# Optimization experiments

Measured on AMD Instinct MI355X. Metric: run time of the kernel, lower is better.

The kernel has to match this reference:

```python
import jax, jax.numpy as jnp
import numpy as np

T, B = 1024, 256
N = T * B
D = 128  # d_model
IN = 36  # lstm input size = 16 + 4 + 16


def _w(k, shape, s=0.1):
    return jax.random.normal(k, shape, dtype=jnp.float32) * s


def setup_inputs() -> dict:
    key = jax.random.key(0)
    ks = jax.random.split(key, 32)
    inp = {}
    inp["image"] = jax.random.uniform(ks[0], (N, 1, 3, 3), jnp.float32) * 255.0
    inp["location"] = jax.random.uniform(ks[1], (N, 2), jnp.float32) * 5.0
    inp["message"] = jax.random.randint(ks[2], (N,), 0, 16)
    inp["done"] = (jax.random.uniform(ks[3], (N,)) < 0.05).astype(jnp.float32)
    inp["h0"] = jax.random.normal(ks[4], (1, B, D), jnp.float32)
    inp["c0"] = jax.random.normal(ks[5], (1, B, D), jnp.float32)
    # visual encoder: 9 -> 256 -> 256 -> 128 -> 16 (ReLU each)
    inp["vis_W1"] = _w(ks[6], (256, 9));   inp["vis_b1"] = jnp.zeros((256,), jnp.float32)
    inp["vis_W2"] = _w(ks[7], (256, 256)); inp["vis_b2"] = jnp.zeros((256,), jnp.float32)
    inp["vis_W3"] = _w(ks[8], (128, 256)); inp["vis_b3"] = jnp.zeros((128,), jnp.float32)
    inp["vis_W4"] = _w(ks[9], (16, 128));  inp["vis_b4"] = jnp.zeros((16,), jnp.float32)
    # location encoder: 2 -> 4
    inp["loc_W"] = _w(ks[10], (4, 2)); inp["loc_b"] = jnp.zeros((4,), jnp.float32)
    # message encoder: Embedding(16,16) -> Linear(16,16) -> ReLU
    inp["emb"] = _w(ks[11], (16, 16), 1.0)
    inp["msg_W"] = _w(ks[12], (16, 16)); inp["msg_b"] = jnp.zeros((16,), jnp.float32)
    # LSTM params (torch layout, gate order i,f,g,o)
    inp["W_ih"] = _w(ks[13], (4 * D, IN)); inp["W_hh"] = _w(ks[14], (4 * D, D))
    inp["b_ih"] = jnp.zeros((4 * D,), jnp.float32); inp["b_hh"] = jnp.zeros((4 * D,), jnp.float32)
    # heads
    inp["actor_W"] = _w(ks[15], (5, D), 0.01);   inp["actor_b"] = jnp.zeros((5,), jnp.float32)
    inp["head_W"] = _w(ks[16], (16, D), 0.01);   inp["head_b"] = jnp.zeros((16,), jnp.float32)
    inp["critic_W"] = _w(ks[17], (1, D), 1.0);   inp["critic_b"] = jnp.zeros((1,), jnp.float32)
    return inp


def reference(image, location, message, done, h0, c0,
              vis_W1, vis_b1, vis_W2, vis_b2, vis_W3, vis_b3, vis_W4, vis_b4,
              loc_W, loc_b, emb, msg_W, msg_b,
              W_ih, W_hh, b_ih, b_hh,
              actor_W, actor_b, head_W, head_b, critic_W, critic_b):
    # encoders (all rows at once)
    x = image.reshape(N, -1) / 255.0
    x = jax.nn.relu(x @ vis_W1.T + vis_b1)
    x = jax.nn.relu(x @ vis_W2.T + vis_b2)
    x = jax.nn.relu(x @ vis_W3.T + vis_b3)
    img_feat = jax.nn.relu(x @ vis_W4.T + vis_b4)                 # [N,16]
    loc_feat = (location / 5.0) @ loc_W.T + loc_b                 # [N,4]
    msg_feat = jax.nn.relu(emb[message] @ msg_W.T + msg_b)        # [N,16]
    feat = jnp.concatenate([img_feat, loc_feat, msg_feat], axis=1).reshape(T, B, IN)
    d = done.reshape(T, B)

    def step(carry, inp_t):
        h, c = carry
        x_t, d_t = inp_t
        m = (1.0 - d_t)[:, None]
        h = h * m
        c = c * m
        gates = x_t @ W_ih.T + h @ W_hh.T + (b_ih + b_hh)         # [B,4D]
        i, f, g, o = jnp.split(gates, 4, axis=-1)
        i = jax.nn.sigmoid(i); f = jax.nn.sigmoid(f)
        g = jnp.tanh(g);       o = jax.nn.sigmoid(o)
        c = f * c + i * g
        h = o * jnp.tanh(c)
        return (h, c), h

    (_, _), hs = jax.lax.scan(step, (h0[0], c0[0]), (feat, d))
    hidden = hs.reshape(N, D)
    action_logits = hidden @ actor_W.T + actor_b                  # [N,5]
    message_logits = hidden @ head_W.T + head_b                   # [N,16]
    value = hidden @ critic_W.T + critic_b                        # [N,1]
    return jnp.concatenate([action_logits, message_logits, value], axis=1)  # [N,22]
```

## Files before the change

kernel.cpp:

```cpp
#include <hip/hip_runtime.h>
#include <hip/hip_bf16.h>

#define DEV __device__ __forceinline__

typedef short short8 __attribute__((ext_vector_type(8)));
typedef _Float16 h8 __attribute__((ext_vector_type(8)));
typedef _Float16 h2 __attribute__((ext_vector_type(2)));
typedef float f32x4 __attribute__((ext_vector_type(4)));
typedef unsigned short u16;

constexpr int T_ = 1024, B_ = 256, N_ = T_ * B_, D_ = 128;
constexpr int FS = 48;
constexpr int NSLOT = 16;
constexpr int SEGQC = 64;
constexpr int MAXIT = 392;
constexpr int CH = 48;
constexpr int WARM = 56;
constexpr int MAXPC = 768;
constexpr unsigned DEADT = 0xFFFFu;
constexpr unsigned TRB = 0x10000u;
constexpr unsigned NWB = 0x20000u;

DEV u16 f2b(float f) {
  unsigned u = __float_as_uint(f);
  return (u16)((u + 0x7fffu + ((u >> 16) & 1u)) >> 16);
}

#if __has_builtin(__builtin_amdgcn_exp2f)
#define EXP2F __builtin_amdgcn_exp2f
#else
#define EXP2F __exp2f
#endif
#if __has_builtin(__builtin_amdgcn_rcpf)
#define RCPF __builtin_amdgcn_rcpf
#else
#define RCPF(x) (1.0f / (x))
#endif
DEV float sigf(float x) { return RCPF(1.0f + EXP2F(x * -1.44269504f)); }
DEV float tanhf_(float x) {
  return fmaf(RCPF(1.0f + EXP2F(x * -2.88539008f)), 2.0f, -1.0f);
}

__global__ void prep_kernel(const float* W1, const float* W2, const float* W3,
                            const float* W4, const float* emb, const float* msgW,
                            const float* msgb, const float* Wih, const float* Whh,
                            const float* bih, const float* bhh, const float* aW,
                            const float* ab, const float* hW, const float* hb,
                            const float* cW, const float* cb, u16* w1p, u16* w2b,
                            u16* w3b, u16* w4b, float* msgtab, _Float16* wfull,
                            float* biass, _Float16* w22, float* b22) {
  int i0 = blockIdx.x * blockDim.x + threadIdx.x;
  int st = gridDim.x * blockDim.x;
  for (int i = i0; i < 256 * 32; i += st) {
    int r = i >> 5, k = i & 31;
    w1p[i] = (k < 9) ? f2b(W1[r * 9 + k]) : (u16)0;
  }
  for (int i = i0; i < 256 * 256; i += st) w2b[i] = f2b(W2[i]);
  for (int i = i0; i < 128 * 256; i += st) w3b[i] = f2b(W3[i]);
  for (int i = i0; i < 16 * 128; i += st) w4b[i] = f2b(W4[i]);
  for (int i = i0; i < 256; i += st) {
    int v = i >> 4, j = i & 15;
    float s = msgb[j];
    for (int k = 0; k < 16; ++k) s += emb[v * 16 + k] * msgW[j * 16 + k];
    msgtab[i] = s > 0.f ? s : 0.f;
  }
  for (int i = i0; i < 512 * 192; i += st) {
    int c = i / 192, k = i % 192;
    float v;
    if (k < 128) v = Whh[(size_t)c * 128 + k];
    else {
      int p = k - 128;
      if (p < 18) v = Wih[(size_t)c * 36 + p];
      else if (p >= 24 && p < 42) v = Wih[(size_t)c * 36 + p - 6];
      else v = 0.f;
    }
    wfull[i] = (_Float16)v;
  }
  for (int i = i0; i < 512; i += st) biass[i] = bih[i] + bhh[i];
  for (int i = i0; i < 32 * 128; i += st) {
    int c = i >> 7, k = i & 127;
    float v = 0.f;
    if (c < 5) v = aW[c * 128 + k];
    else if (c < 21) v = hW[(c - 5) * 128 + k];
    else if (c == 21) v = cW[k];
    w22[i] = (_Float16)v;
  }
  for (int i = i0; i < 32; i += st) {
    float v = 0.f;
    if (i < 5) v = ab[i];
    else if (i < 21) v = hb[i - 5];
    else if (i == 21) v = cb[0];
    b22[i] = v;
  }
}

__global__ __launch_bounds__(64) void seg_scan_kernel(const float* done,
                                                      unsigned* segq, int* nq) {
  __shared__ unsigned short brkpos[1024];
  __shared__ int lcnt[64];
  __shared__ int nb_sh;
  __shared__ int pcs[MAXPC];
  __shared__ int np_sh;
  const int b = blockIdx.x;
  const int l = threadIdx.x;

  unsigned mask = 0;
#pragma unroll
  for (int j = 0; j < 16; ++j) {
    const int t = l * 16 + j;
    const float dv = (t == 0) ? 0.0f : done[(size_t)t * B_ + b];
    mask |= (dv != 0.0f) ? (1u << j) : 0u;
  }
  lcnt[l] = __popc(mask);
  __syncthreads();
  if (l == 0) {
    int acc = 0;
    for (int i = 0; i < 64; ++i) { const int c = lcnt[i]; lcnt[i] = acc; acc += c; }
    nb_sh = acc;
  }
  __syncthreads();
  {
    int off = lcnt[l];
    unsigned mm = mask;
    while (mm) {
      const int j = __builtin_ctz(mm);
      mm &= mm - 1;
      brkpos[off++] = (unsigned short)(l * 16 + j);
    }
  }
  __syncthreads();
  if (l == 0) {
    int np = 0;
    const int nb = nb_sh;
    int t0 = 0;
    for (int s = 0; s <= nb; ++s) {
      const int t1 = (s < nb) ? (int)brkpos[s] : T_;
      int k = 0;
      for (int ps = t0; ps < t1 && np < MAXPC; ps += CH, ++k) {
        const int pl = min(CH, t1 - ps);
        const int wl = (k == 0) ? 0 : min(WARM, ps - t0);
        pcs[np++] = ps | (pl << 10) | (wl << 17);
      }
      t0 = t1;
    }
    np_sh = np;
  }
  __syncthreads();
  const int np = np_sh;
  int ssum[16], scnt[16];
#pragma unroll
  for (int j = 0; j < 16; ++j) { ssum[j] = 0; scnt[j] = 0; }
  if (l == 0 && np > 0) {
    const int e = pcs[0];
    segq[((size_t)b * NSLOT + 0) * SEGQC + 0] = (unsigned)e;
    ssum[0] = ((e >> 10) & 127) + ((e >> 17) & 127);
    scnt[0] = 1;
    pcs[0] = -1;
  }
  __syncthreads();
  for (int it = 1; it < np; ++it) {
    int bestw = -1, bestk = 0;
    for (int j = l; j < np; j += 64) {
      const int e = pcs[j];
      if (e >= 0) {
        const int w = ((e >> 10) & 127) + ((e >> 17) & 127);
        if (w > bestw || (w == bestw && j < bestk)) { bestw = w; bestk = j; }
      }
    }
    int pk = (bestw < 0) ? -1 : ((bestw << 10) | (1023 - bestk));
#pragma unroll
    for (int wd = 32; wd >= 1; wd >>= 1) pk = max(pk, __shfl_xor(pk, wd));
    if (l == 0 && pk >= 0) {
      const int k = 1023 - (pk & 1023);
      const int e = pcs[k];
      const int w = pk >> 10;
      int m = 0, best = 0x7fffffff;
#pragma unroll
      for (int j = 0; j < 16; ++j) {
        const int v = (scnt[j] >= SEGQC) ? 0x7fffffff : ssum[j];
        if (v < best) { best = v; m = j; }
      }
      segq[((size_t)b * NSLOT + m) * SEGQC + scnt[m]] = (unsigned)e;
      ssum[m] += w;
      ++scnt[m];
      pcs[k] = -1;
    }
    __syncthreads();
  }
  if (l == 0) {
#pragma unroll
    for (int j = 0; j < 16; ++j) nq[b * NSLOT + j] = scnt[j];
  }
}

__global__ __launch_bounds__(64) void sched_build_kernel(const unsigned* segq,
                                                         const int* nq,
                                                         unsigned* sched,
                                                         int* bsteps) {
  const int b = blockIdx.x;
  const int l = threadIdx.x;
  int it = 0;
  if (l < NSLOT) {
    const int gs = b * NSLOT + l;
    const unsigned* q = segq + (size_t)gs * SEGQC;
    const int cnt = nq[gs];
    unsigned* sc = sched + (size_t)b * MAXIT * 16 + l;
    for (int s = 0; s < cnt; ++s) {
      const unsigned e = q[s];
      const int ps = (int)(e & 1023u);
      const int pl = (int)((e >> 10) & 127u);
      const int wl = (int)((e >> 17) & 127u);
      for (int j = 0; j < wl && it < MAXIT - 8; ++j) {
        sc[(size_t)it * 16] = (unsigned)(ps - wl + j) | NWB;
        ++it;
      }
      for (int j = 0; j < pl && it < MAXIT - 8; ++j) {
        sc[(size_t)it * 16] = (unsigned)(ps + j) | ((j == pl - 1) ? TRB : 0u);
        ++it;
      }
    }
  }
  int mk = (l < NSLOT) ? it : 0;
#pragma unroll
  for (int w = 8; w >= 1; w >>= 1) mk = max(mk, __shfl_xor(mk, w));
  if (l < NSLOT) {
    unsigned* sc = sched + (size_t)b * MAXIT * 16 + l;
    const int pe = min(mk + 8, MAXIT);
    for (int i2 = it; i2 < pe; ++i2) sc[(size_t)i2 * 16] = DEADT | TRB;
    if (l == 0) bsteps[b] = mk;
  }
}

template <int K, int OUTN, bool SWZIN>
DEV void mlp_layer128(const u16* Ain, u16* Aout, const u16* Wb, const float* bias,
                      int mh, int cq, int lane) {
  constexpr int KT = K / 32;
  constexpr int NT = OUTN / 64;
  constexpr int PASSES = NT / 2;
  const int lr = lane & 15, lg = lane >> 4;
  const int colbase = cq * (OUTN / 4);
  const int rowbase = mh * 64;
#pragma unroll
  for (int ps = 0; ps < PASSES; ++ps) {
    short8 bf[2][KT];
    float bcol[2];
#pragma unroll
    for (int n2 = 0; n2 < 2; ++n2) {
      const int col = colbase + (ps * 2 + n2) * 16 + lr;
#pragma unroll
      for (int kt = 0; kt < KT; ++kt)
        bf[n2][kt] = *(const short8*)(Wb + col * K + kt * 32 + lg * 8);
      bcol[n2] = bias[col];
    }
#pragma unroll
    for (int mt = 0; mt < 4; ++mt) {
      const int arow = rowbase + mt * 16 + lr;
      short8 af[KT];
#pragma unroll
      for (int kt = 0; kt < KT; ++kt) {
        int kb = (kt * 32 + lg * 8) * 2;
        if (SWZIN) kb ^= (arow & 7) << 4;
        af[kt] = *(const short8*)(Ain + arow * K + (kb >> 1));
      }
      f32x4 acc[2];
#pragma unroll
      for (int n2 = 0; n2 < 2; ++n2)
        acc[n2] = f32x4{bcol[n2], bcol[n2], bcol[n2], bcol[n2]};
#pragma unroll
      for (int kt = 0; kt < KT; ++kt)
#pragma unroll
        for (int n2 = 0; n2 < 2; ++n2)
          acc[n2] = __builtin_amdgcn_mfma_f32_16x16x32_bf16(af[kt], bf[n2][kt],
                                                            acc[n2], 0, 0, 0);
#pragma unroll
      for (int n2 = 0; n2 < 2; ++n2) {
        const int col = colbase + (ps * 2 + n2) * 16 + lr;
#pragma unroll
        for (int r = 0; r < 4; ++r) {
          const int orow = rowbase + mt * 16 + lg * 4 + r;
          float v = acc[n2][r];
          v = v > 0.f ? v : 0.f;
          const int kb = (col * 2) ^ ((orow & 7) << 4);
          Aout[orow * OUTN + (kb >> 1)] = f2b(v);
        }
      }
    }
  }
}

__global__ __launch_bounds__(512) void enc_kernel(
    const float* image, const float* location, const int* message,
    const float* vb1, const float* vb2, const float* vb3, const float* vb4,
    const float* locW, const float* locb, const u16* w1p, const u16* w2b,
    const u16* w3b, const u16* w4b, const float* msgtab, _Float16* featf) {
  __shared__ __align__(16) u16 bufA[128 * 256];
  __shared__ __align__(16) u16 bufB[128 * 256];
  const int n0 = blockIdx.x * 128;
  const int tid = threadIdx.x;
  const int wave = tid >> 6, lane = tid & 63;
  const int mh = wave >> 2, cq = wave & 3;

  for (int i = tid; i < 128 * 32; i += 512) {
    int r = i >> 5, k = i & 31;
    float v = (k < 9) ? image[(size_t)(n0 + r) * 9 + k] * (1.0f / 255.0f) : 0.0f;
    bufA[i] = f2b(v);
  }
  __syncthreads();
  mlp_layer128<32, 256, false>(bufA, bufB, w1p, vb1, mh, cq, lane);
  __syncthreads();
  mlp_layer128<256, 256, true>(bufB, bufA, w2b, vb2, mh, cq, lane);
  __syncthreads();
  mlp_layer128<256, 128, true>(bufA, bufB, w3b, vb3, mh, cq, lane);
  __syncthreads();
  {
    const int lr = lane & 15, lg = lane >> 4;
    short8 bfr[4];
#pragma unroll
    for (int kt = 0; kt < 4; ++kt)
      bfr[kt] = *(const short8*)(w4b + lr * 128 + kt * 32 + lg * 8);
    const float bcol = vb4[lr];
    f32x4 acc = {bcol, bcol, bcol, bcol};
#pragma unroll
    for (int kt = 0; kt < 4; ++kt) {
      const int arow = wave * 16 + lr;
      const int kb = ((kt * 32 + lg * 8) * 2) ^ ((arow & 7) << 4);
      const short8 af = *(const short8*)(bufB + arow * 128 + (kb >> 1));
      acc = __builtin_amdgcn_mfma_f32_16x16x32_bf16(af, bfr[kt], acc, 0, 0, 0);
    }
#pragma unroll
    for (int r = 0; r < 4; ++r) {
      const int row = wave * 16 + lg * 4 + r;
      float v = acc[r];
      v = v > 0.f ? v : 0.f;
      featf[(size_t)(n0 + row) * FS + lr] = (_Float16)v;
    }
  }
  if (tid < 128) {
    const int n = n0 + tid;
    _Float16* fr = featf + (size_t)n * FS;
#pragma unroll
    for (int j = 0; j < 6; ++j) fr[18 + j] = (_Float16)0.f;
#pragma unroll
    for (int j = 0; j < 6; ++j) fr[42 + j] = (_Float16)0.f;
    const float x0 = location[(size_t)n * 2] * 0.2f;
    const float x1 = location[(size_t)n * 2 + 1] * 0.2f;
#pragma unroll
    for (int j = 0; j < 4; ++j) {
      const int pos = (j < 2) ? 16 + j : 22 + j;
      fr[pos] = (_Float16)fmaf(x0, locW[j * 2], fmaf(x1, locW[j * 2 + 1], locb[j]));
    }
    const float* mrow = msgtab + message[n] * 16;
#pragma unroll
    for (int j = 0; j < 16; ++j) fr[26 + j] = (_Float16)mrow[j];
  }
}

__global__ __launch_bounds__(512, 2) void lstm_seg_kernel(
    const _Float16* featf, const _Float16* wfull, const float* biass,
    const unsigned* sched, const int* bsteps, const float* h0, const float* c0,
    const float* done, _Float16* hidh) {
  __shared__ __align__(16) char abuf[2][16 * 384];
  const int b = blockIdx.x;
  const int tid = threadIdx.x;
  const int wave = tid >> 6, l = tid & 63;
  const int lc = l & 15, lg = l >> 4;
  const int d = wave * 16 + lc;
  const bool fth = (wave < 6) && (lc < 4);
  const int fslot = lg * 4 + lc;
  const int fch = wave;

  h8 bf[4][6];
#pragma unroll
  for (int g = 0; g < 4; ++g) {
    const _Float16* wp = wfull + (size_t)(g * 128 + d) * 192;
#pragma unroll
    for (int kt = 0; kt < 6; ++kt)
      bf[g][kt] = *(const h8*)(wp + kt * 32 + lg * 8);
  }
  float bias4[4];
#pragma unroll
  for (int g = 0; g < 4; ++g) bias4[g] = biass[g * 128 + d];

  for (int i = tid; i < 2 * 16 * 384 / 4; i += 512) ((float*)abuf)[i] = 0.0f;
  __syncthreads();

  const int nsteps = bsteps[b];
  const unsigned* sb = sched + (size_t)b * MAXIT * 16;
  uint4 sr0 = *(const uint4*)(sb + 0 * 16 + lg * 4);
  uint4 sr1 = *(const uint4*)(sb + 1 * 16 + lg * 4);
  unsigned ss1 = DEADT, ss2 = DEADT, t00 = DEADT;
  if (fth) {
    t00 = sb[0 * 16 + fslot] & 0xFFFFu;
    ss1 = sb[1 * 16 + fslot];
    ss2 = sb[2 * 16 + fslot];
  }

  const float m0 = 1.0f - done[b];
  if (tid < 128)
    *(_Float16*)(abuf[0] + 2 * tid) = (_Float16)(h0[(size_t)b * D_ + tid] * m0);
  float creg[4];
#pragma unroll
  for (int r = 0; r < 4; ++r) {
    const int row = lg * 4 + r;
    creg[r] = (row == 0) ? c0[(size_t)b * D_ + d] * m0 : 0.0f;
  }
  if (fth && t00 != DEADT) {
    const unsigned fo = t00 * (unsigned)(B_ * FS) + (unsigned)(b * FS) + fch * 8;
    const uint4 fz = *(const uint4*)(featf + fo);
    const int byte = (fslot * 384 + 256 + fch * 16) ^ ((fslot & 7) << 4);
    *(uint4*)(abuf[0] + byte) = fz;
  }
  uint4 fvW = {0, 0, 0, 0};
  if (fth && (ss1 & 0xFFFFu) != DEADT) {
    const unsigned fo =
        (ss1 & 0xFFFFu) * (unsigned)(B_ * FS) + (unsigned)(b * FS) + fch * 8;
    fvW = *(const uint4*)(featf + fo);
  }
  __syncthreads();

  int p = 0;
  for (int i = 0; i < nsteps; ++i) {
    const uint4 srN = *(const uint4*)(sb + (size_t)(i + 2) * 16 + lg * 4);
    unsigned ssN = DEADT;
    if (fth) ssN = sb[(size_t)(i + 3) * 16 + fslot];
    const char* bp = abuf[p];
    h8 af[6];
#pragma unroll
    for (int kt = 0; kt < 6; ++kt) {
      const int byte = (lc * 384 + ((kt * 32 + lg * 8) << 1)) ^ ((lc & 7) << 4);
      af[kt] = *(const h8*)(bp + byte);
    }
    uint4 fvN = {0, 0, 0, 0};
    const unsigned t2 = ss2 & 0xFFFFu;
    if (fth && t2 != DEADT) {
      const unsigned fo = t2 * (unsigned)(B_ * FS) + (unsigned)(b * FS) + fch * 8;
      fvN = *(const uint4*)(featf + fo);
    }
    f32x4 acc[4];
#pragma unroll
    for (int g = 0; g < 4; ++g)
      acc[g] = f32x4{bias4[g], bias4[g], bias4[g], bias4[g]};
#pragma unroll
    for (int kt = 0; kt < 6; ++kt)
#pragma unroll
      for (int g = 0; g < 4; ++g)
        acc[g] = __builtin_amdgcn_mfma_f32_16x16x32_f16(af[kt], bf[g][kt],
                                                        acc[g], 0, 0, 0);
    char* bn = abuf[p ^ 1];
#pragma unroll
    for (int r = 0; r < 4; ++r) {
      const int row = lg * 4 + r;
      const unsigned e = ((const unsigned*)&sr0)[r];
      const float gi = sigf(acc[0][r]);
      const float gf = sigf(acc[1][r]);
      const float gg = tanhf_(acc[2][r]);
      const float go = sigf(acc[3][r]);
      const float cn = fmaf(gf, creg[r], gi * gg);
      const float hv = go * tanhf_(cn);
      const unsigned tt = e & 0xFFFFu;
      const bool tr = (e & TRB) != 0u;
      creg[r] = tr ? 0.0f : cn;
      *(_Float16*)(bn + ((row * 384 + 2 * d) ^ ((row & 7) << 4))) =
          (_Float16)(tr ? 0.0f : hv);
      if (tt != DEADT && !(e & NWB)) {
        const unsigned ho = (tt << 15) + (unsigned)((b << 7) + d);
        hidh[ho] = (_Float16)hv;
      }
    }
    if (fth && (ss1 & 0xFFFFu) != DEADT) {
      const int byte = (fslot * 384 + 256 + fch * 16) ^ ((fslot & 7) << 4);
      *(uint4*)(bn + byte) = fvW;
    }
    sr0 = sr1; sr1 = srN;
    ss1 = ss2; ss2 = ssN;
    fvW = fvN;
    asm volatile("s_waitcnt lgkmcnt(0)" ::: "memory");
    __builtin_amdgcn_s_barrier();
    p ^= 1;
  }
}

__global__ __launch_bounds__(256) void head_kernel(const _Float16* hidh,
                                                   const _Float16* w22,
                                                   const float* b22, float* out) {
  const int tid = threadIdx.x;
  const int w = tid >> 6, l = tid & 63;
  const int lr = l & 15, lg = l >> 4;
  const int row0 = blockIdx.x * 64 + w * 16;

  h8 bfr[2][4];
#pragma unroll
  for (int ct = 0; ct < 2; ++ct)
#pragma unroll
    for (int kt = 0; kt < 4; ++kt)
      bfr[ct][kt] = *(const h8*)(w22 + (ct * 16 + lr) * 128 + kt * 32 + lg * 8);
  h8 af[4];
#pragma unroll
  for (int kt = 0; kt < 4; ++kt)
    af[kt] = *(const h8*)(hidh + (size_t)(row0 + lr) * D_ + kt * 32 + lg * 8);

  f32x4 acc[2];
#pragma unroll
  for (int ct = 0; ct < 2; ++ct) acc[ct] = f32x4{0.f, 0.f, 0.f, 0.f};
#pragma unroll
  for (int kt = 0; kt < 4; ++kt)
#pragma unroll
    for (int ct = 0; ct < 2; ++ct)
      acc[ct] = __builtin_amdgcn_mfma_f32_16x16x32_f16(af[kt], bfr[ct][kt],
                                                       acc[ct], 0, 0, 0);
#pragma unroll
  for (int ct = 0; ct < 2; ++ct) {
    const int col = ct * 16 + lr;
    if (col < 22) {
      const float bb = b22[col];
#pragma unroll
      for (int r = 0; r < 4; ++r) {
        const int row = row0 + lg * 4 + r;
        out[(size_t)row * 22 + col] = acc[ct][r] + bb;
      }
    }
  }
}

extern "C" void kernel_launch(void* const* d_in, const int* in_sizes, int n_in,
                              void* d_out, int out_size, void* d_ws, size_t ws_size,
                              hipStream_t stream) {
  const float* image = (const float*)d_in[0];
  const float* location = (const float*)d_in[1];
  const int* message = (const int*)d_in[2];
  const float* done = (const float*)d_in[3];
  const float* h0 = (const float*)d_in[4];
  const float* c0 = (const float*)d_in[5];
  const float* vW1 = (const float*)d_in[6];
  const float* vb1 = (const float*)d_in[7];
  const float* vW2 = (const float*)d_in[8];
  const float* vb2 = (const float*)d_in[9];
  const float* vW3 = (const float*)d_in[10];
  const float* vb3 = (const float*)d_in[11];
  const float* vW4 = (const float*)d_in[12];
  const float* vb4 = (const float*)d_in[13];
  const float* locW = (const float*)d_in[14];
  const float* locb = (const float*)d_in[15];
  const float* emb = (const float*)d_in[16];
  const float* msgW = (const float*)d_in[17];
  const float* msgb = (const float*)d_in[18];
  const float* Wih = (const float*)d_in[19];
  const float* Whh = (const float*)d_in[20];
  const float* bih = (const float*)d_in[21];
  const float* bhh = (const float*)d_in[22];
  const float* aW = (const float*)d_in[23];
  const float* ab = (const float*)d_in[24];
  const float* hW = (const float*)d_in[25];
  const float* hb = (const float*)d_in[26];
  const float* cW = (const float*)d_in[27];
  const float* cb = (const float*)d_in[28];

  char* ws = (char*)d_ws;
  size_t off = 0;
  auto alloc = [&](size_t bytes) {
    void* p = ws + off;
    off = (off + bytes + 255) & ~(size_t)255;
    return p;
  };
  _Float16* featf = (_Float16*)alloc((size_t)N_ * FS * 2);
  _Float16* hidh = (_Float16*)alloc((size_t)N_ * D_ * 2);
  u16* w1p = (u16*)alloc(256 * 32 * 2);
  u16* w2b = (u16*)alloc(256 * 256 * 2);
  u16* w3b = (u16*)alloc(128 * 256 * 2);
  u16* w4b = (u16*)alloc(16 * 128 * 2);
  float* msgtab = (float*)alloc(256 * 4);
  _Float16* wfull = (_Float16*)alloc(512 * 192 * 2);
  float* biass = (float*)alloc(512 * 4);
  unsigned* segq = (unsigned*)alloc((size_t)B_ * NSLOT * SEGQC * 4);
  int* nqA = (int*)alloc(B_ * NSLOT * 4);
  unsigned* sched = (unsigned*)alloc((size_t)B_ * MAXIT * 16 * 4);
  int* bsteps = (int*)alloc(B_ * 4);
  _Float16* w22 = (_Float16*)alloc(32 * 128 * 2);
  float* b22 = (float*)alloc(32 * 4);
  (void)in_sizes; (void)n_in; (void)out_size; (void)ws_size;

  prep_kernel<<<128, 256, 0, stream>>>(vW1, vW2, vW3, vW4, emb, msgW, msgb, Wih,
                                       Whh, bih, bhh, aW, ab, hW, hb, cW, cb, w1p,
                                       w2b, w3b, w4b, msgtab, wfull, biass, w22,
                                       b22);
  seg_scan_kernel<<<B_, 64, 0, stream>>>(done, segq, nqA);
  sched_build_kernel<<<B_, 64, 0, stream>>>(segq, nqA, sched, bsteps);
  enc_kernel<<<N_ / 128, 512, 0, stream>>>(image, location, message, vb1, vb2, vb3,
                                           vb4, locW, locb, w1p, w2b, w3b, w4b,
                                           msgtab, featf);
  lstm_seg_kernel<<<B_, 512, 0, stream>>>(featf, wfull, biass, sched, bsteps,
                                          h0, c0, done, hidh);
  head_kernel<<<N_ / 64, 256, 0, stream>>>(hidh, w22, b22, (float*)d_out);
}
```

Baseline: 483.6 us.

## Split visual encoder into two kernels with chunked global intermediate

The single 512-thread encoder kernel, which used 128 KB of LDS per block, is split into two 256-thread kernels over 64-row tiles. Layers 1-2 write a bf16 activation buffer to global memory and layers 3-4 read it back, with the work processed in chunks sized to fit the workspace. The image 1/255 scaling is also folded into the first-layer weights. The aim is to cut LDS per block so more blocks fit per CU, at the cost of an extra global round trip for the 256-wide activations and more kernel launches.

```diff
diff --git a/kernel.cpp b/kernel.cpp
--- a/kernel.cpp
+++ b/kernel.cpp
@@ -53,7 +53,7 @@
   int st = gridDim.x * blockDim.x;
   for (int i = i0; i < 256 * 32; i += st) {
     int r = i >> 5, k = i & 31;
-    w1p[i] = (k < 9) ? f2b(W1[r * 9 + k]) : (u16)0;
+    w1p[i] = (k < 9) ? f2b(W1[r * 9 + k] * (1.0f / 255.0f)) : (u16)0;
   }
   for (int i = i0; i < 256 * 256; i += st) w2b[i] = f2b(W2[i]);
   for (int i = i0; i < 128 * 256; i += st) w3b[i] = f2b(W3[i]);
@@ -232,14 +232,12 @@
 }
 
 template <int K, int OUTN, bool SWZIN>
-DEV void mlp_layer128(const u16* Ain, u16* Aout, const u16* Wb, const float* bias,
-                      int mh, int cq, int lane) {
+DEV void mlp_layer64(const u16* Ain, u16* Aout, const u16* Wb, const float* bias,
+                     int cq, int lane) {
   constexpr int KT = K / 32;
-  constexpr int NT = OUTN / 64;
-  constexpr int PASSES = NT / 2;
+  constexpr int PASSES = OUTN / 128;
   const int lr = lane & 15, lg = lane >> 4;
   const int colbase = cq * (OUTN / 4);
-  const int rowbase = mh * 64;
 #pragma unroll
   for (int ps = 0; ps < PASSES; ++ps) {
     short8 bf[2][KT];
@@ -254,7 +252,7 @@
     }
 #pragma unroll
     for (int mt = 0; mt < 4; ++mt) {
-      const int arow = rowbase + mt * 16 + lr;
+      const int arow = mt * 16 + lr;
       short8 af[KT];
 #pragma unroll
       for (int kt = 0; kt < KT; ++kt) {
@@ -277,7 +275,7 @@
         const int col = colbase + (ps * 2 + n2) * 16 + lr;
 #pragma unroll
         for (int r = 0; r < 4; ++r) {
-          const int orow = rowbase + mt * 16 + lg * 4 + r;
+          const int orow = mt * 16 + lg * 4 + r;
           float v = acc[n2][r];
           v = v > 0.f ? v : 0.f;
           const int kb = (col * 2) ^ ((orow & 7) << 4);
@@ -288,29 +286,54 @@
   }
 }
 
-__global__ __launch_bounds__(512) void enc_kernel(
-    const float* image, const float* location, const int* message,
-    const float* vb1, const float* vb2, const float* vb3, const float* vb4,
-    const float* locW, const float* locb, const u16* w1p, const u16* w2b,
-    const u16* w3b, const u16* w4b, const float* msgtab, _Float16* featf) {
-  __shared__ __align__(16) u16 bufA[128 * 256];
-  __shared__ __align__(16) u16 bufB[128 * 256];
-  const int n0 = blockIdx.x * 128;
+__global__ __launch_bounds__(256) void enc12_kernel(const float* image,
+                                                    const u16* w1p, const float* vb1,
+                                                    const u16* w2b, const float* vb2,
+                                                    u16* a2, int n0base) {
+  __shared__ __align__(16) u16 sx[64 * 32];
+  __shared__ __align__(16) u16 b1[64 * 256];
+  __shared__ __align__(16) u16 b2[64 * 256];
+  const int nloc = blockIdx.x * 64;
+  const int n0 = n0base + nloc;
   const int tid = threadIdx.x;
-  const int wave = tid >> 6, lane = tid & 63;
-  const int mh = wave >> 2, cq = wave & 3;
-
-  for (int i = tid; i < 128 * 32; i += 512) {
+  const int cq = tid >> 6, lane = tid & 63;
+
+  for (int i = tid; i < 64 * 32; i += 256) {
     int r = i >> 5, k = i & 31;
-    float v = (k < 9) ? image[(size_t)(n0 + r) * 9 + k] * (1.0f / 255.0f) : 0.0f;
-    bufA[i] = f2b(v);
-  }
-  __syncthreads();
-  mlp_layer128<32, 256, false>(bufA, bufB, w1p, vb1, mh, cq, lane);
-  __syncthreads();
-  mlp_layer128<256, 256, true>(bufB, bufA, w2b, vb2, mh, cq, lane);
-  __syncthreads();
-  mlp_layer128<256, 128, true>(bufA, bufB, w3b, vb3, mh, cq, lane);
+    sx[i] = (k < 9) ? f2b(image[(size_t)(n0 + r) * 9 + k]) : (u16)0;
+  }
+  __syncthreads();
+  mlp_layer64<32, 256, false>(sx, b1, w1p, vb1, cq, lane);
+  __syncthreads();
+  mlp_layer64<256, 256, true>(b1, b2, w2b, vb2, cq, lane);
+  __syncthreads();
+  for (int i = tid; i < 64 * 32; i += 256) {
+    const int row = i >> 5, c8 = i & 31;
+    const int byte = (row * 512 + c8 * 16) ^ ((row & 7) << 4);
+    const short8 v = *(const short8*)((const char*)b2 + byte);
+    *(short8*)(a2 + (size_t)(nloc + row) * 256 + c8 * 8) = v;
+  }
+}
+
+__global__ __launch_bounds__(256) void enc34_kernel(
+    const u16* a2, const float* location, const int* message, const u16* w3b,
+    const float* vb3, const u16* w4b, const float* vb4, const float* locW,
+    const float* locb, const float* msgtab, _Float16* featf, int n0base) {
+  __shared__ __align__(16) u16 b1[64 * 256];
+  __shared__ __align__(16) u16 b2[64 * 128];
+  const int nloc = blockIdx.x * 64;
+  const int n0 = n0base + nloc;
+  const int tid = threadIdx.x;
+  const int cq = tid >> 6, lane = tid & 63;
+
+  for (int i = tid; i < 64 * 32; i += 256) {
+    const int row = i >> 5, c8 = i & 31;
+    const short8 v = *(const short8*)(a2 + (size_t)(nloc + row) * 256 + c8 * 8);
+    const int byte = (row * 512 + c8 * 16) ^ ((row & 7) << 4);
+    *(short8*)((char*)b1 + byte) = v;
+  }
+  __syncthreads();
+  mlp_layer64<256, 128, true>(b1, b2, w3b, vb3, cq, lane);
   __syncthreads();
   {
     const int lr = lane & 15, lg = lane >> 4;
@@ -322,20 +345,20 @@
     f32x4 acc = {bcol, bcol, bcol, bcol};
 #pragma unroll
     for (int kt = 0; kt < 4; ++kt) {
-      const int arow = wave * 16 + lr;
+      const int arow = cq * 16 + lr;
       const int kb = ((kt * 32 + lg * 8) * 2) ^ ((arow & 7) << 4);
-      const short8 af = *(const short8*)(bufB + arow * 128 + (kb >> 1));
+      const short8 af = *(const short8*)(b2 + arow * 128 + (kb >> 1));
       acc = __builtin_amdgcn_mfma_f32_16x16x32_bf16(af, bfr[kt], acc, 0, 0, 0);
     }
 #pragma unroll
     for (int r = 0; r < 4; ++r) {
-      const int row = wave * 16 + lg * 4 + r;
+      const int row = cq * 16 + lg * 4 + r;
       float v = acc[r];
       v = v > 0.f ? v : 0.f;
       featf[(size_t)(n0 + row) * FS + lr] = (_Float16)v;
     }
   }
-  if (tid < 128) {
+  if (tid < 64) {
     const int n = n0 + tid;
     _Float16* fr = featf + (size_t)n * FS;
 #pragma unroll
@@ -577,7 +600,13 @@
   int* bsteps = (int*)alloc(B_ * 4);
   _Float16* w22 = (_Float16*)alloc(32 * 128 * 2);
   float* b22 = (float*)alloc(32 * 4);
-  (void)in_sizes; (void)n_in; (void)out_size; (void)ws_size;
+  int nchunk = 32;
+  for (int c = 2; c <= 32; c *= 2) {
+    if (off + (size_t)(N_ / c) * 256 * 2 + 256 <= ws_size) { nchunk = c; break; }
+  }
+  const int crows = N_ / nchunk;
+  u16* a2 = (u16*)alloc((size_t)crows * 256 * 2);
+  (void)in_sizes; (void)n_in; (void)out_size;
 
   prep_kernel<<<128, 256, 0, stream>>>(vW1, vW2, vW3, vW4, emb, msgW, msgb, Wih,
                                        Whh, bih, bhh, aW, ab, hW, hb, cW, cb, w1p,
@@ -585,9 +614,14 @@
                                        b22);
   seg_scan_kernel<<<B_, 64, 0, stream>>>(done, segq, nqA);
   sched_build_kernel<<<B_, 64, 0, stream>>>(segq, nqA, sched, bsteps);
-  enc_kernel<<<N_ / 128, 512, 0, stream>>>(image, location, message, vb1, vb2, vb3,
-                                           vb4, locW, locb, w1p, w2b, w3b, w4b,
-                                           msgtab, featf);
+  for (int c = 0; c < nchunk; ++c) {
+    const int n0 = c * crows;
+    enc12_kernel<<<crows / 64, 256, 0, stream>>>(image, w1p, vb1, w2b, vb2, a2,
+                                                 n0);
+    enc34_kernel<<<crows / 64, 256, 0, stream>>>(a2, location, message, w3b, vb3,
+                                                 w4b, vb4, locW, locb, msgtab,
+                                                 featf, n0);
+  }
   lstm_seg_kernel<<<B_, 512, 0, stream>>>(featf, wfull, biass, sched, bsteps,
                                           h0, c0, done, hidh);
   head_kernel<<<N_ / 64, 256, 0, stream>>>(hidh, w22, b22, (float*)d_out);
```

Result: slower. 505.3 us (+4.5%).
